# Kernel optimization log

Hardware: AMD Instinct MI355X
Metric: run time of the kernel (lower is better)

Reference implementation:

```python
import jax, jax.numpy as jnp
import numpy as np

SR = 44100
S_TAUS = [10.0, 50.0, 100.0]   # ms
L_TAUS = [500.0, 1500.0, 3000.0]  # ms
EPS = 1e-8


def ms2coef(ms, sr):
    return float(1.0 - np.exp(-2200.0 / (ms * sr)))


def ema(x, coef):
    # First-order leaky integrator y[t] = coef*x[t] + (1-coef)*y[t-1], y[-1]=0.
    # x: [B, T]; scan over time with carry of shape [B].
    coef = jnp.asarray(coef, x.dtype)
    one_m = jnp.asarray(1.0, x.dtype) - coef

    def step(carry, xt):
        y = coef * xt + one_m * carry
        return y, y

    _, ys = jax.lax.scan(step, jnp.zeros(x.shape[0], x.dtype), x.T)
    return ys.T  # [B, T]


def hadamard(x):
    # mid/side transform on channel dim (-2), orthonormal scaling
    m = x[..., 0, :] + x[..., 1, :]
    s = x[..., 0, :] - x[..., 1, :]
    return jnp.stack([m, s], axis=-2) * jnp.asarray(np.sqrt(0.5), x.dtype)


def ldr_feat(x_sq, s_coef, l_coef, shift):
    # log short-term envelope minus (time-aligned) log long-term envelope
    short = jnp.log(ema(x_sq, s_coef))
    long_ = jnp.log(ema(x_sq, l_coef))
    return short - jnp.roll(long_, -shift, axis=-1)


def setup_inputs() -> dict:
    key = jax.random.key(0)
    k1, k2 = jax.random.split(key)
    x_pred = jax.random.normal(k1, (4, 2, 1048576), dtype=jnp.float32)
    x_true = jax.random.normal(k2, (4, 2, 1048576), dtype=jnp.float32)
    return {"x_pred": x_pred, "x_true": x_true}


def reference(x_pred, x_true):
    xp = hadamard(x_pred)
    xt = hadamard(x_true)
    T = xp.shape[-1]
    ps = jnp.clip(jnp.square(xp), EPS, None).reshape(-1, T)
    ts = jnp.clip(jnp.square(xt), EPS, None).reshape(-1, T)
    total = jnp.asarray(0.0, x_pred.dtype)
    for s_ms, l_ms in zip(S_TAUS, L_TAUS):
        sc = ms2coef(s_ms, SR)
        lc = ms2coef(l_ms, SR)
        shift = int(SR * (l_ms - s_ms) * 0.0005)
        fp = ldr_feat(ps, sc, lc, shift)
        ft = ldr_feat(ts, sc, lc, shift)
        total = total + jnp.mean(jnp.abs(fp - ft))
    return total
```

## Files before the change

### kernel.cpp

```cpp
#include <hip/hip_runtime.h>
#include <cmath>


#define T_LEN    1048576
#define CHUNKS   256
#define CLEN     4096
#define NT1      256
#define SEG1     16
#define COLS     65536
#define JMAX     65535
#define EPS_CLIP 1e-8f
#define K2SEG    32
#define K2NSEG   8

struct K1Args {
  float d[6];
  float apw[6][7];
};
struct K2Args {
  float dL[6];
  float dL32[6];
};
struct CarryPack {
  float d[3];
  float apw[3][9];
};

__device__ __constant__ const int D_SHIFT[3] = {10804, 31972, 63945};

__global__ __launch_bounds__(NT1)
void k1_stage(const float* __restrict__ xp, const float* __restrict__ xt,
              float* __restrict__ Eloc, float* __restrict__ Bs,
              float* __restrict__ Bl, int mode, K1Args ka)
{
  int chunk = blockIdx.x, b = blockIdx.y;
  int which = b >> 2, sig = b & 3, tid = threadIdx.x;
  long base = (long)chunk * CLEN + (long)tid * SEG1;
  const float* x0 = (which ? xt : xp) + (long)sig * 2 * T_LEN;
  const float* x1 = x0 + T_LEN;

  float S[12];
#pragma unroll
  for (int j = 0; j < 12; j++) S[j] = 0.f;

#pragma unroll
  for (int i = 0; i < SEG1 / 4; i++) {
    float4 a = *(const float4*)(x0 + base + 4*i);
    float4 c4 = *(const float4*)(x1 + base + 4*i);
    float sm, sp, pm, ps;
#define STEP(CMP) \
    sm = a.CMP + c4.CMP; sp = a.CMP - c4.CMP; \
    pm = fmaxf(0.5f * sm * sm, EPS_CLIP); ps = fmaxf(0.5f * sp * sp, EPS_CLIP); \
    _Pragma("unroll") \
    for (int cf = 0; cf < 6; cf++) { \
      S[cf*2+0] = fmaf(ka.d[cf], S[cf*2+0], pm); \
      S[cf*2+1] = fmaf(ka.d[cf], S[cf*2+1], ps); \
    }
    STEP(x) STEP(y) STEP(z) STEP(w)
#undef STEP
  }

  int lane = tid & 63, w = tid >> 6;
#pragma unroll
  for (int i = 0; i < 6; i++) {
#pragma unroll
    for (int j = 0; j < 12; j++) {
      float up = __shfl_up(S[j], 1u << i, 64);
      if (lane >= (1 << i)) S[j] = fmaf(ka.apw[j >> 1][i], up, S[j]);
    }
  }
  __shared__ float WT[4][12];
  if (lane == 63)
#pragma unroll
    for (int j = 0; j < 12; j++) WT[w][j] = S[j];
  __syncthreads();
  float C[12];
#pragma unroll
  for (int j = 0; j < 12; j++) C[j] = 0.f;
#pragma unroll
  for (int i = 0; i < 4; i++) {
    if (i < w) {
#pragma unroll
      for (int j = 0; j < 12; j++)
        C[j] = fmaf(ka.apw[j >> 1][6], C[j], WT[i][j]);
    }
  }
  float alp[6];
#pragma unroll
  for (int cf = 0; cf < 6; cf++) {
    int e = lane + 1;
    float a = 1.f;
#pragma unroll
    for (int i = 0; i < 7; i++)
      if (e & (1 << i)) a *= ka.apw[cf][i];
    alp[cf] = a;
  }
#pragma unroll
  for (int j = 0; j < 12; j++) S[j] = fmaf(alp[j >> 1], C[j], S[j]);

  long col = (long)chunk * (CLEN / SEG1) + tid;
  if (mode & 2) {
#pragma unroll
    for (int k = 0; k < 3; k++)
#pragma unroll
      for (int st2 = 0; st2 < 2; st2++)
        Bs[(long)(4*k + which*2 + st2) * (4L*COLS) + (long)sig*COLS + col] = S[4*k + st2];
  }
  if (mode & 1) {
#pragma unroll
    for (int k = 0; k < 3; k++)
#pragma unroll
      for (int st2 = 0; st2 < 2; st2++)
        Bl[(long)(4*k + which*2 + st2) * (4L*COLS) + (long)sig*COLS + col] = S[4*k + 2 + st2];
  }
  if (mode != 2 && tid == NT1 - 1) {
#pragma unroll
    for (int cf = 0; cf < 6; cf++)
#pragma unroll
      for (int st = 0; st < 2; st++)
        Eloc[chunk * 96 + (which*8 + sig*2 + st) * 6 + cf] = S[cf*2 + st];
  }
}

__global__ __launch_bounds__(768)
void k2_scan(const float* __restrict__ Eloc, float* __restrict__ Y, K2Args ka)
{
  int col = threadIdx.x;
  int seg = threadIdx.y;
  float dL = ka.dL[col % 6];
  float A  = ka.dL32[col % 6];
  int c0 = seg * K2SEG;

  float yloc[K2SEG];
  float y = 0.f;
#pragma unroll
  for (int i = 0; i < K2SEG; i++) {
    y = fmaf(dL, y, Eloc[(c0 + i) * 96 + col]);
    yloc[i] = y;
  }

  __shared__ float SY[K2NSEG][96];
  SY[seg][col] = y;
  __syncthreads();

  float C = 0.f;
  for (int s = 0; s < seg; s++) C = fmaf(A, C, SY[s][col]);

  float w = dL;
#pragma unroll
  for (int i = 0; i < K2SEG; i++) {
    Y[(c0 + i) * 96 + col] = fmaf(w, C, yloc[i]);
    w *= dL;
  }
}

__global__ __launch_bounds__(256)
void k3_table(const float* __restrict__ Bl, const float* __restrict__ Y,
              float* __restrict__ Etab, CarryPack cp)
{
  int chunk = blockIdx.x, sig = blockIdx.y, tid = threadIdx.x;
  long col = (long)chunk * 256 + tid;

  float Yc[12];
#pragma unroll
  for (int j = 0; j < 12; j++) Yc[j] = 0.f;
  if (chunk > 0) {
    const float* Yp = Y + (chunk - 1) * 96;
    int rm = sig * 2;
#pragma unroll
    for (int k = 0; k < 3; k++) {
      int cf = 2*k + 1;
      Yc[4*k+0] = Yp[rm*6 + cf];       Yc[4*k+1] = Yp[(rm+1)*6 + cf];
      Yc[4*k+2] = Yp[(8+rm)*6 + cf];   Yc[4*k+3] = Yp[(8+rm+1)*6 + cf];
    }
  }
  float fac[3];
#pragma unroll
  for (int k = 0; k < 3; k++) {
    int e = tid + 1;
    float a = 1.f;
#pragma unroll
    for (int i = 0; i < 9; i++)
      if (e & (1 << i)) a *= cp.apw[k][i];
    fac[k] = a;
  }
#pragma unroll
  for (int k = 0; k < 3; k++) {
    float y0 = fmaf(fac[k], Yc[4*k+0], Bl[(long)(4*k+0)*(4L*COLS) + (long)sig*COLS + col]);
    float y1 = fmaf(fac[k], Yc[4*k+1], Bl[(long)(4*k+1)*(4L*COLS) + (long)sig*COLS + col]);
    float y2 = fmaf(fac[k], Yc[4*k+2], Bl[(long)(4*k+2)*(4L*COLS) + (long)sig*COLS + col]);
    float y3 = fmaf(fac[k], Yc[4*k+3], Bl[(long)(4*k+3)*(4L*COLS) + (long)sig*COLS + col]);
    float em = __log2f(y0) - __log2f(y2);
    float es = __log2f(y1) - __log2f(y3);
    long rowm = (long)(k*8 + sig*2);
    Etab[rowm * COLS + col] = em;
    Etab[(rowm+1) * COLS + col] = es;
  }
}

__device__ __forceinline__ float slow_lerp(const float* __restrict__ row, int q)
{
  int qm = q - 15;
  if (qm < 0) return row[0];
  int j = qm >> 4;
  if (j >= JMAX) return row[JMAX];
  float f = (float)(qm & 15) * 0.0625f;
  float a = row[j], b = row[j + 1];
  return fmaf(f, b - a, a);
}

__global__ __launch_bounds__(256)
void k4all(const float* __restrict__ xp, const float* __restrict__ xt,
           const float* __restrict__ Y, const float* __restrict__ Bs,
           const float* __restrict__ Etab, float* __restrict__ part, CarryPack cp)
{
  int chunk = blockIdx.x, sig = blockIdx.y, tid = threadIdx.x;
  long col = (long)chunk * 256 + tid;
  long base = col * 16;

  float Yc[12];
#pragma unroll
  for (int j = 0; j < 12; j++) Yc[j] = 0.f;
  if (chunk > 0) {
    const float* Yp = Y + (chunk - 1) * 96;
    int rm = sig * 2;
#pragma unroll
    for (int k = 0; k < 3; k++) {
      int cf = 2*k;
      Yc[4*k+0] = Yp[rm*6 + cf];       Yc[4*k+1] = Yp[(rm+1)*6 + cf];
      Yc[4*k+2] = Yp[(8+rm)*6 + cf];   Yc[4*k+3] = Yp[(8+rm+1)*6 + cf];
    }
  }
  float y[12];
  if (tid == 0) {
#pragma unroll
    for (int j = 0; j < 12; j++) y[j] = Yc[j];
  } else {
    float fac[3];
#pragma unroll
    for (int k = 0; k < 3; k++) {
      float a = 1.f;
#pragma unroll
      for (int i = 0; i < 8; i++)
        if (tid & (1 << i)) a *= cp.apw[k][i];
      fac[k] = a;
    }
#pragma unroll
    for (int k = 0; k < 3; k++)
#pragma unroll
      for (int q = 0; q < 4; q++)
        y[4*k+q] = fmaf(fac[k], Yc[4*k+q],
                        Bs[(long)(4*k+q)*(4L*COLS) + (long)sig*COLS + (col-1)]);
  }

  float tm0[3], tm1[3], tm2[3], ts0[3], ts1[3], ts2[3];
  int ofs[3], q0a[3]; bool fastp[3];
#pragma unroll
  for (int k = 0; k < 3; k++) {
    int q0 = (int)base + D_SHIFT[k]; if (q0 >= T_LEN) q0 -= T_LEN;
    q0a[k] = q0;
    int qm = q0 - 15;
    bool f = (qm >= 0) && ((qm >> 4) <= JMAX - 2);
    fastp[k] = f;
    const float* Tm = Etab + (long)(k * 8 + sig * 2) * COLS;
    const float* Ts = Tm + COLS;
    int j0 = f ? (qm >> 4) : 0;
    ofs[k] = f ? (qm & 15) : 0;
    tm0[k] = Tm[j0]; tm1[k] = Tm[j0 + 1]; tm2[k] = Tm[j0 + 2];
    ts0[k] = Ts[j0]; ts1[k] = Ts[j0 + 1]; ts2[k] = Ts[j0 + 2];
  }

  const float* p0 = xp + (long)sig * 2 * T_LEN;
  const float* p1 = p0 + T_LEN;
  const float* t0 = xt + (long)sig * 2 * T_LEN;
  const float* t1 = t0 + T_LEN;

  float acc0 = 0.f, acc1 = 0.f;
#pragma unroll
  for (int qt = 0; qt < 4; qt++) {
    float4 a4 = *(const float4*)(p0 + base + 4*qt);
    float4 b4 = *(const float4*)(p1 + base + 4*qt);
    float4 u4 = *(const float4*)(t0 + base + 4*qt);
    float4 w4 = *(const float4*)(t1 + base + 4*qt);
#define SAMP(CI, CMP) { \
      const int m = 4*qt + CI; \
      float sm = a4.CMP + b4.CMP, sd = a4.CMP - b4.CMP; \
      float pm = fmaxf(0.5f*sm*sm, EPS_CLIP), ps = fmaxf(0.5f*sd*sd, EPS_CLIP); \
      float em_ = u4.CMP + w4.CMP, ed_ = u4.CMP - w4.CMP; \
      float qm_ = fmaxf(0.5f*em_*em_, EPS_CLIP), qs_ = fmaxf(0.5f*ed_*ed_, EPS_CLIP); \
      _Pragma("unroll") \
      for (int k = 0; k < 3; k++) { \
        float dd = cp.d[k]; \
        y[4*k+0] = fmaf(dd, y[4*k+0], pm);  y[4*k+1] = fmaf(dd, y[4*k+1], ps); \
        y[4*k+2] = fmaf(dd, y[4*k+2], qm_); y[4*k+3] = fmaf(dd, y[4*k+3], qs_); \
        float Dm = __log2f(y[4*k+0]) - __log2f(y[4*k+2]); \
        float Ds = __log2f(y[4*k+1]) - __log2f(y[4*k+3]); \
        float em, es; \
        if (fastp[k]) { \
          int d0 = ofs[k] + m; \
          bool hi = d0 >= 16; \
          float am = hi ? tm1[k] : tm0[k], bm = hi ? tm2[k] : tm1[k]; \
          float as = hi ? ts1[k] : ts0[k], bs = hi ? ts2[k] : ts1[k]; \
          float f = (float)(d0 - (hi ? 16 : 0)) * 0.0625f; \
          em = fmaf(f, bm - am, am); \
          es = fmaf(f, bs - as, as); \
        } else { \
          int q = q0a[k] + m; if (q >= T_LEN) q -= T_LEN; \
          const float* Tm = Etab + (long)(k * 8 + sig * 2) * COLS; \
          em = slow_lerp(Tm, q); \
          es = slow_lerp(Tm + COLS, q); \
        } \
        acc0 += fabsf(Dm - em); \
        acc1 += fabsf(Ds - es); \
      } \
    }
    SAMP(0,x) SAMP(1,y) SAMP(2,z) SAMP(3,w)
#undef SAMP
  }

  float acc = acc0 + acc1;
#pragma unroll
  for (int off = 32; off > 0; off >>= 1) acc += __shfl_down(acc, off, 64);
  __shared__ float psum[4];
  int lane = tid & 63, w = tid >> 6;
  if (lane == 0) psum[w] = acc;
  __syncthreads();
  if (tid == 0)
    part[sig * CHUNKS + chunk] = psum[0] + psum[1] + psum[2] + psum[3];
}

__global__ void k5_final(const float* __restrict__ part, float* __restrict__ out)
{
  __shared__ double lds[256];
  int tid = threadIdx.x;
  double s = 0.0;
  for (int i = tid; i < 4 * CHUNKS; i += 256) s += (double)part[i];
  lds[tid] = s; __syncthreads();
  for (int o = 128; o > 0; o >>= 1) {
    if (tid < o) lds[tid] += lds[tid + o];
    __syncthreads();
  }
  if (tid == 0)
    out[0] = (float)(lds[0] * (0.6931471805599453 / (8.0 * 1048576.0)));
}

extern "C" void kernel_launch(void* const* d_in, const int* in_sizes, int n_in,
                              void* d_out, int out_size, void* d_ws, size_t ws_size,
                              hipStream_t stream)
{
  (void)in_sizes; (void)n_in; (void)out_size;
  const float* xp = (const float*)d_in[0];
  const float* xt = (const float*)d_in[1];
  float* out = (float*)d_out;
  char* ws = (char*)d_ws;

  const size_t OFF_ELOC = 0;
  const size_t OFF_Y    = 98304;
  const size_t OFF_PART = 196608;
  const size_t OFF_ETAB = 212992;
  const size_t OFF_B    = 6504448;
  const size_t HALF_B   = 12L * 4 * COLS * 4;
  const size_t NEED_FULL = OFF_B + 2 * HALF_B;
  float* Eloc = (float*)(ws + OFF_ELOC);
  float* Ybuf = (float*)(ws + OFF_Y);
  float* part = (float*)(ws + OFF_PART);
  float* Etab = (float*)(ws + OFF_ETAB);
  float* Bsh  = (float*)(ws + OFF_B);
  float* Blo  = (float*)(ws + OFF_B + HALF_B);

  static const double S_MS[3] = {10.0, 50.0, 100.0};
  static const double L_MS[3] = {500.0, 1500.0, 3000.0};

  K1Args k1a; K2Args k2a; CarryPack cpS, cpL;
  for (int k = 0; k < 3; k++) {
    for (int which = 0; which < 2; which++) {
      int idx = 2 * k + which;
      double ms = which ? L_MS[k] : S_MS[k];
      float cF = (float)(1.0 - std::exp(-2200.0 / (ms * 44100.0)));
      float dF = 1.0f - cF;
      k1a.d[idx] = dF;
      double a16 = std::pow((double)dF, 16.0);
      for (int i = 0; i < 7; i++)
        k1a.apw[idx][i] = (float)std::pow(a16, (double)(1 << i));
      k2a.dL[idx]   = (float)std::pow((double)dF, (double)CLEN);
      k2a.dL32[idx] = (float)std::pow((double)dF, (double)CLEN * (double)K2SEG);
      CarryPack& cp = which ? cpL : cpS;
      cp.d[k] = dF;
      for (int i = 0; i < 9; i++)
        cp.apw[k][i] = (float)std::pow(a16, (double)(1 << i));
    }
  }

  bool full = (ws_size >= NEED_FULL);
  if (full) {
    k1_stage<<<dim3(CHUNKS, 8), NT1, 0, stream>>>(xp, xt, Eloc, Bsh, Blo, 3, k1a);
    k2_scan<<<dim3(1), dim3(96, K2NSEG), 0, stream>>>(Eloc, Ybuf, k2a);
    k3_table<<<dim3(CHUNKS, 4), 256, 0, stream>>>(Blo, Ybuf, Etab, cpL);
    k4all<<<dim3(CHUNKS, 4), 256, 0, stream>>>(xp, xt, Ybuf, Bsh, Etab, part, cpS);
  } else {
    k1_stage<<<dim3(CHUNKS, 8), NT1, 0, stream>>>(xp, xt, Eloc, Bsh, Bsh, 1, k1a);
    k2_scan<<<dim3(1), dim3(96, K2NSEG), 0, stream>>>(Eloc, Ybuf, k2a);
    k3_table<<<dim3(CHUNKS, 4), 256, 0, stream>>>(Bsh, Ybuf, Etab, cpL);
    k1_stage<<<dim3(CHUNKS, 8), NT1, 0, stream>>>(xp, xt, Eloc, Bsh, Bsh, 2, k1a);
    k4all<<<dim3(CHUNKS, 4), 256, 0, stream>>>(xp, xt, Ybuf, Bsh, Etab, part, cpS);
  }
  k5_final<<<1, 256, 0, stream>>>(part, out);
}
```

Measured before the change: 141.9 us.

## Fuse all stages into one cooperative persistent kernel with grid syncs

Replaces the five separate kernel launches with a single cooperative kernel that loops blocks over each stage's work units and separates stages with grid-wide syncs. The carry scan between stages becomes a serial loop over 256 chunks run by 96 threads of one block, replacing the two-level segmented scan. This aims to remove launch gaps and the tail of each stage. In exchange, grid syncs add their own cost, occupancy is capped by launch bounds, and the serial scan lengthens the critical path.

New measurement: 295.2 us. 2.08x slower.

```diff
diff --git a/kernel.cpp b/kernel.cpp
--- a/kernel.cpp
+++ b/kernel.cpp
@@ -1,5 +1,8 @@
 #include <hip/hip_runtime.h>
+#include <hip/hip_cooperative_groups.h>
 #include <cmath>
+
+namespace cg = cooperative_groups;
 
 
 #define T_LEN    1048576
@@ -28,13 +31,11 @@
 
 __device__ __constant__ const int D_SHIFT[3] = {10804, 31972, 63945};
 
-__global__ __launch_bounds__(NT1)
-void k1_stage(const float* __restrict__ xp, const float* __restrict__ xt,
-              float* __restrict__ Eloc, float* __restrict__ Bs,
-              float* __restrict__ Bl, int mode, K1Args ka)
-{
-  int chunk = blockIdx.x, b = blockIdx.y;
-  int which = b >> 2, sig = b & 3, tid = threadIdx.x;
+__device__ __forceinline__ void k1_body(const float* __restrict__ xp, const float* __restrict__ xt,
+    float* __restrict__ Eloc, float* __restrict__ Bs, float* __restrict__ Bl,
+    int mode, const K1Args& ka, int chunk, int b, int tid, float (*WT)[12])
+{
+  int which = b >> 2, sig = b & 3;
   long base = (long)chunk * CLEN + (long)tid * SEG1;
   const float* x0 = (which ? xt : xp) + (long)sig * 2 * T_LEN;
   const float* x1 = x0 + T_LEN;
@@ -69,7 +70,6 @@
       if (lane >= (1 << i)) S[j] = fmaf(ka.apw[j >> 1][i], up, S[j]);
     }
   }
-  __shared__ float WT[4][12];
   if (lane == 63)
 #pragma unroll
     for (int j = 0; j < 12; j++) WT[w][j] = S[j];
@@ -122,43 +122,9 @@
   }
 }
 
-__global__ __launch_bounds__(768)
-void k2_scan(const float* __restrict__ Eloc, float* __restrict__ Y, K2Args ka)
-{
-  int col = threadIdx.x;
-  int seg = threadIdx.y;
-  float dL = ka.dL[col % 6];
-  float A  = ka.dL32[col % 6];
-  int c0 = seg * K2SEG;
-
-  float yloc[K2SEG];
-  float y = 0.f;
-#pragma unroll
-  for (int i = 0; i < K2SEG; i++) {
-    y = fmaf(dL, y, Eloc[(c0 + i) * 96 + col]);
-    yloc[i] = y;
-  }
-
-  __shared__ float SY[K2NSEG][96];
-  SY[seg][col] = y;
-  __syncthreads();
-
-  float C = 0.f;
-  for (int s = 0; s < seg; s++) C = fmaf(A, C, SY[s][col]);
-
-  float w = dL;
-#pragma unroll
-  for (int i = 0; i < K2SEG; i++) {
-    Y[(c0 + i) * 96 + col] = fmaf(w, C, yloc[i]);
-    w *= dL;
-  }
-}
-
-__global__ __launch_bounds__(256)
-void k3_table(const float* __restrict__ Bl, const float* __restrict__ Y,
-              float* __restrict__ Etab, CarryPack cp)
-{
-  int chunk = blockIdx.x, sig = blockIdx.y, tid = threadIdx.x;
+__device__ __forceinline__ void k3_body(const float* __restrict__ Bl, const float* __restrict__ Y,
+    float* __restrict__ Etab, const CarryPack& cp, int chunk, int sig, int tid)
+{
   long col = (long)chunk * 256 + tid;
 
   float Yc[12];
@@ -209,12 +175,11 @@
   return fmaf(f, b - a, a);
 }
 
-__global__ __launch_bounds__(256)
-void k4all(const float* __restrict__ xp, const float* __restrict__ xt,
-           const float* __restrict__ Y, const float* __restrict__ Bs,
-           const float* __restrict__ Etab, float* __restrict__ part, CarryPack cp)
-{
-  int chunk = blockIdx.x, sig = blockIdx.y, tid = threadIdx.x;
+__device__ __forceinline__ void k4_body(const float* __restrict__ xp, const float* __restrict__ xt,
+    const float* __restrict__ Y, const float* __restrict__ Bs,
+    const float* __restrict__ Etab, float* __restrict__ part,
+    const CarryPack& cp, int chunk, int sig, int tid, float* psum)
+{
   long col = (long)chunk * 256 + tid;
   long base = col * 16;
 
@@ -321,12 +286,120 @@
   float acc = acc0 + acc1;
 #pragma unroll
   for (int off = 32; off > 0; off >>= 1) acc += __shfl_down(acc, off, 64);
-  __shared__ float psum[4];
   int lane = tid & 63, w = tid >> 6;
   if (lane == 0) psum[w] = acc;
   __syncthreads();
   if (tid == 0)
     part[sig * CHUNKS + chunk] = psum[0] + psum[1] + psum[2] + psum[3];
+}
+
+__global__ __launch_bounds__(256, 2)
+void fused(const float* __restrict__ xp, const float* __restrict__ xt,
+           float* __restrict__ Eloc, float* __restrict__ Y,
+           float* __restrict__ Bs, float* __restrict__ Bl,
+           float* __restrict__ Etab, float* __restrict__ part,
+           float* __restrict__ out,
+           K1Args ka, K2Args k2a, CarryPack cpL, CarryPack cpS)
+{
+  cg::grid_group grid = cg::this_grid();
+  __shared__ float WT[4][12];
+  __shared__ float psum[4];
+  __shared__ double dsum[256];
+  int tid = threadIdx.x, bid = blockIdx.x, nb = gridDim.x;
+
+  for (int u = bid; u < 2048; u += nb) {
+    k1_body(xp, xt, Eloc, Bs, Bl, 3, ka, u >> 3, u & 7, tid, WT);
+    __syncthreads();
+  }
+  grid.sync();
+
+  if (bid == 0 && tid < 96) {
+    float dL = k2a.dL[tid % 6];
+    float yv = 0.f;
+#pragma unroll 8
+    for (int c = 0; c < CHUNKS; c++) {
+      yv = fmaf(dL, yv, Eloc[c * 96 + tid]);
+      Y[c * 96 + tid] = yv;
+    }
+  }
+  grid.sync();
+
+  for (int u = bid; u < 1024; u += nb) {
+    k3_body(Bl, Y, Etab, cpL, u >> 2, u & 3, tid);
+  }
+  grid.sync();
+
+  for (int u = bid; u < 1024; u += nb) {
+    k4_body(xp, xt, Y, Bs, Etab, part, cpS, u >> 2, u & 3, tid, psum);
+    __syncthreads();
+  }
+  grid.sync();
+
+  if (bid == 0) {
+    double s = 0.0;
+    for (int i = tid; i < 4 * CHUNKS; i += 256) s += (double)part[i];
+    dsum[tid] = s; __syncthreads();
+    for (int o = 128; o > 0; o >>= 1) {
+      if (tid < o) dsum[tid] += dsum[tid + o];
+      __syncthreads();
+    }
+    if (tid == 0)
+      out[0] = (float)(dsum[0] * (0.6931471805599453 / (8.0 * 1048576.0)));
+  }
+}
+
+__global__ __launch_bounds__(NT1)
+void k1_stage(const float* __restrict__ xp, const float* __restrict__ xt,
+              float* __restrict__ Eloc, float* __restrict__ Bs,
+              float* __restrict__ Bl, int mode, K1Args ka)
+{
+  __shared__ float WT[4][12];
+  k1_body(xp, xt, Eloc, Bs, Bl, mode, ka, blockIdx.x, blockIdx.y, threadIdx.x, WT);
+}
+
+__global__ __launch_bounds__(768)
+void k2_scan(const float* __restrict__ Eloc, float* __restrict__ Y, K2Args ka)
+{
+  int col = threadIdx.x;
+  int seg = threadIdx.y;
+  float dL = ka.dL[col % 6];
+  float A  = ka.dL32[col % 6];
+  int c0 = seg * K2SEG;
+
+  float yloc[K2SEG];
+  float y = 0.f;
+#pragma unroll
+  for (int i = 0; i < K2SEG; i++) {
+    y = fmaf(dL, y, Eloc[(c0 + i) * 96 + col]);
+    yloc[i] = y;
+  }
+  __shared__ float SY[K2NSEG][96];
+  SY[seg][col] = y;
+  __syncthreads();
+  float C = 0.f;
+  for (int s = 0; s < seg; s++) C = fmaf(A, C, SY[s][col]);
+  float w = dL;
+#pragma unroll
+  for (int i = 0; i < K2SEG; i++) {
+    Y[(c0 + i) * 96 + col] = fmaf(w, C, yloc[i]);
+    w *= dL;
+  }
+}
+
+__global__ __launch_bounds__(256)
+void k3_table(const float* __restrict__ Bl, const float* __restrict__ Y,
+              float* __restrict__ Etab, CarryPack cp)
+{
+  k3_body(Bl, Y, Etab, cp, blockIdx.x, blockIdx.y, threadIdx.x);
+}
+
+__global__ __launch_bounds__(256)
+void k4all(const float* __restrict__ xp, const float* __restrict__ xt,
+           const float* __restrict__ Y, const float* __restrict__ Bs,
+           const float* __restrict__ Etab, float* __restrict__ part, CarryPack cp)
+{
+  __shared__ float psum[4];
+  k4_body(xp, xt, Y, Bs, Etab, part, cp, blockIdx.x, blockIdx.y, threadIdx.x, psum);
 }
 
 __global__ void k5_final(const float* __restrict__ part, float* __restrict__ out)
@@ -392,17 +465,37 @@
   }
 
   bool full = (ws_size >= NEED_FULL);
+  bool done = false;
+
   if (full) {
-    k1_stage<<<dim3(CHUNKS, 8), NT1, 0, stream>>>(xp, xt, Eloc, Bsh, Blo, 3, k1a);
-    k2_scan<<<dim3(1), dim3(96, K2NSEG), 0, stream>>>(Eloc, Ybuf, k2a);
-    k3_table<<<dim3(CHUNKS, 4), 256, 0, stream>>>(Blo, Ybuf, Etab, cpL);
-    k4all<<<dim3(CHUNKS, 4), 256, 0, stream>>>(xp, xt, Ybuf, Bsh, Etab, part, cpS);
-  } else {
-    k1_stage<<<dim3(CHUNKS, 8), NT1, 0, stream>>>(xp, xt, Eloc, Bsh, Bsh, 1, k1a);
-    k2_scan<<<dim3(1), dim3(96, K2NSEG), 0, stream>>>(Eloc, Ybuf, k2a);
-    k3_table<<<dim3(CHUNKS, 4), 256, 0, stream>>>(Bsh, Ybuf, Etab, cpL);
-    k1_stage<<<dim3(CHUNKS, 8), NT1, 0, stream>>>(xp, xt, Eloc, Bsh, Bsh, 2, k1a);
-    k4all<<<dim3(CHUNKS, 4), 256, 0, stream>>>(xp, xt, Ybuf, Bsh, Etab, part, cpS);
-  }
-  k5_final<<<1, 256, 0, stream>>>(part, out);
-}
+    int maxB = 0;
+    hipError_t qe = hipOccupancyMaxActiveBlocksPerMultiprocessor(&maxB, fused, 256, 0);
+    if (qe == hipSuccess && maxB > 0) {
+      int grid = maxB * 256;
+      if (grid > 1024) grid = 1024;
+      void* args[] = {(void*)&xp, (void*)&xt, (void*)&Eloc, (void*)&Ybuf,
+                      (void*)&Bsh, (void*)&Blo, (void*)&Etab, (void*)&part,
+                      (void*)&out, (void*)&k1a, (void*)&k2a, (void*)&cpL,
+                      (void*)&cpS};
+      hipError_t le = hipLaunchCooperativeKernel((const void*)fused, dim3(grid),
+                                                 dim3(256), args, 0, stream);
+      if (le == hipSuccess) done = true;
+    }
+  }
+
+  if (!done) {
+    if (full) {
+      k1_stage<<<dim3(CHUNKS, 8), NT1, 0, stream>>>(xp, xt, Eloc, Bsh, Blo, 3, k1a);
+      k2_scan<<<dim3(1), dim3(96, K2NSEG), 0, stream>>>(Eloc, Ybuf, k2a);
+      k3_table<<<dim3(CHUNKS, 4), 256, 0, stream>>>(Blo, Ybuf, Etab, cpL);
+      k4all<<<dim3(CHUNKS, 4), 256, 0, stream>>>(xp, xt, Ybuf, Bsh, Etab, part, cpS);
+    } else {
+      k1_stage<<<dim3(CHUNKS, 8), NT1, 0, stream>>>(xp, xt, Eloc, Bsh, Bsh, 1, k1a);
+      k2_scan<<<dim3(1), dim3(96, K2NSEG), 0, stream>>>(Eloc, Ybuf, k2a);
+      k3_table<<<dim3(CHUNKS, 4), 256, 0, stream>>>(Bsh, Ybuf, Etab, cpL);
+      k1_stage<<<dim3(CHUNKS, 8), NT1, 0, stream>>>(xp, xt, Eloc, Bsh, Bsh, 2, k1a);
+      k4all<<<dim3(CHUNKS, 4), 256, 0, stream>>>(xp, xt, Ybuf, Bsh, Etab, part, cpS);
+    }
+    k5_final<<<1, 256, 0, stream>>>(part, out);
+  }
+}
```
